# Performance work log

Hardware: AMD Instinct MI355X
Metric: run time of the kernel (lower is better)

## Reference

```python
import jax, jax.numpy as jnp
import numpy as np

N = 100000   # nodes
E = 1600000  # edges
D_IN = 7
H1 = 64
H2 = 32
G = 64       # graphs in batch


def setup_inputs() -> dict:
    key = jax.random.key(0)
    ks = jax.random.split(key, 10)
    x = jax.random.normal(ks[0], (N, D_IN), jnp.float32)
    edge_index = jax.random.randint(ks[1], (2, E), 0, N, dtype=jnp.int64)
    batch = jnp.sort(jax.random.randint(ks[2], (N,), 0, G, dtype=jnp.int64))
    # Glorot-style init for GCN weights
    W1 = jax.random.normal(ks[3], (D_IN, H1), jnp.float32) * (1.0 / np.sqrt(D_IN))
    b1 = jnp.zeros((H1,), jnp.float32)
    W2 = jax.random.normal(ks[4], (H1, H2), jnp.float32) * (1.0 / np.sqrt(H1))
    b2 = jnp.zeros((H2,), jnp.float32)
    W3 = jax.random.normal(ks[5], (H1, H2), jnp.float32) * (1.0 / np.sqrt(H1))
    b3 = jnp.zeros((H2,), jnp.float32)
    eps = jax.random.normal(ks[6], (N, H2), jnp.float32)  # reparam noise
    return dict(x=x, edge_index=edge_index, batch=batch,
                W1=W1, b1=b1, W2=W2, b2=b2, W3=W3, b3=b3, eps=eps)


def _gcn_agg(xw, src, dst, dis):
    # Symmetric-normalized aggregation with self-loops (PyG GCNConv default):
    # out[i] = sum_{(j->i)} d_i^{-1/2} d_j^{-1/2} xw[j] + d_i^{-1} xw[i]
    norm = (dis[src] * dis[dst])[:, None]
    msg = xw[src] * norm                      # [E, H] gather
    out = jax.ops.segment_sum(msg, dst, num_segments=N)  # scatter-add
    return out + xw * (dis * dis)[:, None]    # self-loop term


def reference(x, edge_index, batch, W1, b1, W2, b2, W3, b3, eps):
    src, dst = edge_index[0], edge_index[1]
    # degree on A + I (targets), unit edge weights
    deg = jax.ops.segment_sum(jnp.ones((E,), x.dtype), dst, num_segments=N) + 1.0
    dis = jax.lax.rsqrt(deg)  # deg^{-1/2}

    hidden1 = jax.nn.relu(_gcn_agg(x @ W1, src, dst, dis) + b1)

    # global mean pool of raw x over graphs
    counts = jax.ops.segment_sum(jnp.ones((N,), x.dtype), batch, num_segments=G)
    x_pooled = jax.ops.segment_sum(x, batch, num_segments=G) / jnp.maximum(counts, 1.0)[:, None]

    mu = jax.nn.relu(_gcn_agg(hidden1 @ W2, src, dst, dis) + b2)
    logvar = jax.nn.relu(_gcn_agg(hidden1 @ W3, src, dst, dis) + b3)

    # reparameterize: std = exp(logvar) (no 0.5 factor, as in source)
    z = eps * jnp.exp(logvar) + mu
    return z, x_pooled, mu, logvar
```

## Files before the change

### kernel.cpp

```cpp
#include <hip/hip_runtime.h>
#include <hip/hip_bf16.h>
#include <hip/hip_fp16.h>

#define NN 100000
#define NE 1600000
#define D_IN 7
#define H1 64
#define H2 32
#define NG 64
#define TE 2048
#define NTILE 782
#define BSH 9
#define NBUK 196
#define CAP 10240

typedef _Float16 f16x8 __attribute__((ext_vector_type(8)));
typedef float f32x4 __attribute__((ext_vector_type(4)));

__device__ int lower_bound_i(const int* a, int n, int v) {
    int lo = 0, hi = n;
    while (lo < hi) { int mid = (lo + hi) >> 1; if (a[mid] < v) lo = mid + 1; else hi = mid; }
    return lo;
}

__global__ void k_pi(const float* __restrict__ x, const int* __restrict__ batch,
                     float* __restrict__ outp, int* __restrict__ bucket_cursor) {
    int g = blockIdx.x, t = threadIdx.x;
    if (g == NG) {
        if (t < 256) bucket_cursor[t] = t * CAP;
        return;
    }
    __shared__ int bounds[2];
    __shared__ float red[256 * D_IN];
    if (t == 0) {
        bounds[0] = lower_bound_i(batch, NN, g);
        bounds[1] = lower_bound_i(batch, NN, g + 1);
    }
    __syncthreads();
    int s = bounds[0], e = bounds[1];
    float acc[D_IN];
#pragma unroll
    for (int k = 0; k < D_IN; k++) acc[k] = 0.f;
    for (int n = s + t; n < e; n += 256) {
#pragma unroll
        for (int k = 0; k < D_IN; k++) acc[k] += x[n * D_IN + k];
    }
#pragma unroll
    for (int k = 0; k < D_IN; k++) red[t * D_IN + k] = acc[k];
    __syncthreads();
    if (t < D_IN) {
        float sum = 0.f;
        for (int i = 0; i < 256; i++) sum += red[i * D_IN + t];
        float cnt = (float)(e - s);
        outp[g * D_IN + t] = sum / fmaxf(cnt, 1.f);
    }
}

__global__ __launch_bounds__(256) void k_bin(const int* __restrict__ src,
                                             const int* __restrict__ dst,
                                             int* __restrict__ bucket_cursor,
                                             int* __restrict__ staging) {
    __shared__ int hist[NBUK];
    __shared__ int startx[NBUK];
    __shared__ int runb[NBUK];
    __shared__ int cur[NBUK];
    __shared__ int wsum[4];
    __shared__ int2 pairs[TE];
    int t = threadIdx.x;
    int base = blockIdx.x * TE;
    int tile_cnt = min(TE, NE - base);
    for (int i = t; i < NBUK; i += 256) hist[i] = 0;
    __syncthreads();
    int myd[TE / 256], mys[TE / 256];
#pragma unroll
    for (int k = 0; k < TE / 256; k++) {
        int i = base + k * 256 + t;
        if (i < NE) {
            myd[k] = dst[i]; mys[k] = src[i];
            atomicAdd(&hist[myd[k] >> BSH], 1);
        } else myd[k] = -1;
    }
    __syncthreads();
    int hv = (t < NBUK) ? hist[t] : 0;
    int lane = t & 63, wv = t >> 6;
    int sv = hv;
#pragma unroll
    for (int off = 1; off < 64; off <<= 1) {
        int n = __shfl_up(sv, off, 64);
        if (lane >= off) sv += n;
    }
    if (lane == 63) wsum[wv] = sv;
    __syncthreads();
    int wbase = 0;
#pragma unroll
    for (int i = 0; i < 4; i++) wbase += (i < wv) ? wsum[i] : 0;
    if (t < NBUK) {
        int ex = wbase + sv - hv;
        startx[t] = ex;
        cur[t] = ex;
        if (hv > 0) runb[t] = atomicAdd(&bucket_cursor[t], hv);
    }
    __syncthreads();
#pragma unroll
    for (int k = 0; k < TE / 256; k++) {
        if (myd[k] >= 0) {
            int b = myd[k] >> BSH;
            int slot = atomicAdd(&cur[b], 1);
            pairs[slot] = make_int2(myd[k], mys[k]);
        }
    }
    __syncthreads();
    for (int i = t; i < tile_cnt; i += 256) {
        int2 p = pairs[i];
        int b = p.x >> BSH;
        staging[runb[b] + (i - startx[b])] = ((p.x & 511) << 17) | p.y;
    }
}

__global__ __launch_bounds__(512) void k_build(const int* __restrict__ staging,
                                               const int* __restrict__ bucket_cursor,
                                               int2* __restrict__ rowinfo,
                                               float* __restrict__ dis,
                                               int* __restrict__ csr,
                                               const float* __restrict__ x,
                                               float* __restrict__ xd8) {
    __shared__ int cnt[512];
    __shared__ int cur[512];
    __shared__ int wsum[8];
    int t = threadIdx.x;
    int nbase = blockIdx.x << BSH;
    int ebase = blockIdx.x * CAP;
    int eend = bucket_cursor[blockIdx.x];
    cnt[t] = 0;
    __syncthreads();
    for (int i = ebase + t; i < eend; i += 512)
        atomicAdd(&cnt[staging[i] >> 17], 1);
    __syncthreads();
    int v = cnt[t];
    int lane = t & 63, wv = t >> 6;
    int sv = v;
#pragma unroll
    for (int off = 1; off < 64; off <<= 1) {
        int n = __shfl_up(sv, off, 64);
        if (lane >= off) sv += n;
    }
    if (lane == 63) wsum[wv] = sv;
    __syncthreads();
    int wbase = 0;
#pragma unroll
    for (int i = 0; i < 8; i++) wbase += (i < wv) ? wsum[i] : 0;
    int excl = wbase + sv - v;
    cur[t] = excl;
    int node = nbase + t;
    if (node < NN) {
        rowinfo[node] = make_int2(ebase + excl, v);
        float d = rsqrtf((float)v + 1.0f);
        dis[node] = d;
        const float* xr = x + (size_t)node * D_IN;
        float4 w0 = make_float4(d * xr[0], d * xr[1], d * xr[2], d * xr[3]);
        float4 w1 = make_float4(d * xr[4], d * xr[5], d * xr[6], 0.f);
        float4* xo = (float4*)(xd8 + (size_t)node * 8);
        xo[0] = w0; xo[1] = w1;
    }
    __syncthreads();
    for (int i = ebase + t; i < eend; i += 512) {
        int p = staging[i];
        int pos = ebase + atomicAdd(&cur[p >> 17], 1);
        csr[pos] = p & 0x1FFFF;
    }
}

__global__ __launch_bounds__(256) void k_aggx(const int2* __restrict__ rowinfo,
                                              const float* __restrict__ dis,
                                              const int* __restrict__ csr,
                                              const float* __restrict__ xd8,
                                              const float* __restrict__ W1,
                                              const float* __restrict__ b1,
                                              __half* __restrict__ h1h) {
    __shared__ float sW[D_IN * H1];
    __shared__ float sb[H1];
    __shared__ float sAx[64 * 9];
    int t = threadIdx.x;
    for (int i = t; i < D_IN * H1; i += 256) sW[i] = W1[i];
    if (t < H1) sb[t] = b1[t];
    int ll = t & 3;
    int ln = t >> 2;
    int node = blockIdx.x * 64 + ln;
    int nodec = min(node, NN - 1);
    int2 ri = rowinfo[nodec];
    int start = ri.x, c = ri.y;
    int cpos = start + max(c - 1, 0);
    int cmax = c;
    cmax = max(cmax, __shfl_xor(cmax, 4, 64));
    cmax = max(cmax, __shfl_xor(cmax, 8, 64));
    cmax = max(cmax, __shfl_xor(cmax, 16, 64));
    cmax = max(cmax, __shfl_xor(cmax, 32, 64));
    const float2* xb = (const float2*)xd8;
    float2 acc[4];
#pragma unroll
    for (int k = 0; k < 4; k++) acc[k] = make_float2(0.f, 0.f);
    for (int j = 0; j < cmax; j += 16) {
#pragma unroll
        for (int k = 0; k < 16; k++) {
            bool v = (j + k) < c;
            int s = csr[min(start + j + k, cpos)];
            s = v ? s : nodec;
            float2 r = xb[(size_t)s * 4 + ll];
            acc[k & 3].x += v ? r.x : 0.f;
            acc[k & 3].y += v ? r.y : 0.f;
        }
    }
    float sx = acc[0].x + acc[1].x + acc[2].x + acc[3].x;
    float sy = acc[0].y + acc[1].y + acc[2].y + acc[3].y;
    float2 self = xb[(size_t)nodec * 4 + ll];
    float dn = dis[nodec];
    sAx[ln * 9 + 2 * ll]     = dn * (sx + self.x);
    sAx[ln * 9 + 2 * ll + 1] = dn * (sy + self.y);
    __syncthreads();
    if (node < NN) {
        const float* axp = &sAx[ln * 9];
        union { __half h[16]; float4 f[2]; } u;
#pragma unroll
        for (int j = 0; j < 16; j++) {
            int h = ll * 16 + j;
            float a = sb[h];
#pragma unroll
            for (int k = 0; k < D_IN; k++) a += axp[k] * sW[k * H1 + h];
            u.h[j] = __float2half(dn * fmaxf(a, 0.f));
        }
        float4* d4 = (float4*)(h1h + (size_t)node * H1 + ll * 16);
        d4[0] = u.f[0];
        d4[1] = u.f[1];
    }
}

__device__ __forceinline__ void pk_acc4(__half2* a, float4 r, bool v) {
    unsigned u0 = v ? *reinterpret_cast<unsigned*>(&r.x) : 0u;
    unsigned u1 = v ? *reinterpret_cast<unsigned*>(&r.y) : 0u;
    unsigned u2 = v ? *reinterpret_cast<unsigned*>(&r.z) : 0u;
    unsigned u3 = v ? *reinterpret_cast<unsigned*>(&r.w) : 0u;
    a[0] = __hadd2(a[0], *reinterpret_cast<__half2*>(&u0));
    a[1] = __hadd2(a[1], *reinterpret_cast<__half2*>(&u1));
    a[2] = __hadd2(a[2], *reinterpret_cast<__half2*>(&u2));
    a[3] = __hadd2(a[3], *reinterpret_cast<__half2*>(&u3));
}

__global__ __launch_bounds__(256) void k_agg2f(const int2* __restrict__ rowinfo,
                                               const float* __restrict__ dis,
                                               const int* __restrict__ csr,
                                               const __half* __restrict__ h1h,
                                               const float* __restrict__ W2,
                                               const float* __restrict__ W3,
                                               const float* __restrict__ b2,
                                               const float* __restrict__ b3,
                                               const float* __restrict__ eps,
                                               float* __restrict__ out_z,
                                               float* __restrict__ out_mu,
                                               float* __restrict__ out_lv) {
    __shared__ __align__(16) _Float16 sW[64 * 80];
    __shared__ __align__(16) _Float16 sT[64 * 72];
    int t = threadIdx.x;
    for (int i = t; i < 64 * 64; i += 256) {
        int c = i >> 6, k = i & 63;
        float w = (c < 32) ? W2[k * H2 + c] : W3[k * H2 + (c - 32)];
        sW[c * 80 + k] = (_Float16)w;
    }
    int lane = t & 63;
    int wv = t >> 6;
    int l7 = lane & 7, sub8 = lane >> 3;
    const float4* yb4 = (const float4*)h1h;
    for (int g = 0; g < 2; g++) {
        int lrow = wv * 16 + g * 8 + sub8;
        int node = blockIdx.x * 64 + lrow;
        int nodec = min(node, NN - 1);
        int2 ri = rowinfo[nodec];
        int start = ri.x, c = ri.y;
        int cpos = start + max(c - 1, 0);
        int cmax = c;
        cmax = max(cmax, __shfl_xor(cmax, 8, 64));
        cmax = max(cmax, __shfl_xor(cmax, 16, 64));
        cmax = max(cmax, __shfl_xor(cmax, 32, 64));
        __half2 z2 = __float2half2_rn(0.f);
        __half2 acc[4][4];
#pragma unroll
        for (int i = 0; i < 4; i++)
#pragma unroll
            for (int k = 0; k < 4; k++) acc[i][k] = z2;
        for (int j = 0; j < cmax; j += 16) {
#pragma unroll
            for (int k = 0; k < 16; k++) {
                bool v = (j + k) < c;
                int s = csr[min(start + j + k, cpos)];
                s = v ? s : nodec;
                float4 r = yb4[(size_t)s * 8 + l7];
                pk_acc4(acc[k & 3], r, v);
            }
        }
        __half2 s0 = __hadd2(__hadd2(acc[0][0], acc[1][0]), __hadd2(acc[2][0], acc[3][0]));
        __half2 s1 = __hadd2(__hadd2(acc[0][1], acc[1][1]), __hadd2(acc[2][1], acc[3][1]));
        __half2 s2 = __hadd2(__hadd2(acc[0][2], acc[1][2]), __hadd2(acc[2][2], acc[3][2]));
        __half2 s3 = __hadd2(__hadd2(acc[0][3], acc[1][3]), __hadd2(acc[2][3], acc[3][3]));
        float4 selfv = yb4[(size_t)nodec * 8 + l7];
        __half2* sh = reinterpret_cast<__half2*>(&selfv);
        float dn = dis[nodec];
        float2 f0 = __half22float2(s0), e0 = __half22float2(sh[0]);
        float2 f1 = __half22float2(s1), e1 = __half22float2(sh[1]);
        float2 f2 = __half22float2(s2), e2 = __half22float2(sh[2]);
        float2 f3 = __half22float2(s3), e3 = __half22float2(sh[3]);
        __half2 o0, o1, o2, o3;
        o0.x = __float2half(dn * (f0.x + e0.x)); o0.y = __float2half(dn * (f0.y + e0.y));
        o1.x = __float2half(dn * (f1.x + e1.x)); o1.y = __float2half(dn * (f1.y + e1.y));
        o2.x = __float2half(dn * (f2.x + e2.x)); o2.y = __float2half(dn * (f2.y + e2.y));
        o3.x = __float2half(dn * (f3.x + e3.x)); o3.y = __float2half(dn * (f3.y + e3.y));
        float4 st;
        st.x = *reinterpret_cast<float*>(&o0);
        st.y = *reinterpret_cast<float*>(&o1);
        st.z = *reinterpret_cast<float*>(&o2);
        st.w = *reinterpret_cast<float*>(&o3);
        *(float4*)&sT[lrow * 72 + l7 * 8] = st;
    }
    __syncthreads();
    int sub = lane >> 4, l15 = lane & 15;
    int c15 = l15, k8 = sub;
    const _Float16* ap = &sT[(wv * 16 + c15) * 72];
    f16x8 a0 = *(const f16x8*)(ap + k8 * 8);
    f16x8 a1 = *(const f16x8*)(ap + 32 + k8 * 8);
    const _Float16* wb = sW + (size_t)c15 * 80 + k8 * 8;
    f16x8 b00 = *(const f16x8*)(wb);
    f16x8 b01 = *(const f16x8*)(wb + 32);
    f16x8 b10 = *(const f16x8*)(wb + 16 * 80);
    f16x8 b11 = *(const f16x8*)(wb + 16 * 80 + 32);
    f16x8 b20 = *(const f16x8*)(wb + 32 * 80);
    f16x8 b21 = *(const f16x8*)(wb + 32 * 80 + 32);
    f16x8 b30 = *(const f16x8*)(wb + 48 * 80);
    f16x8 b31 = *(const f16x8*)(wb + 48 * 80 + 32);
    f32x4 ac0 = {0.f, 0.f, 0.f, 0.f};
    f32x4 ac1 = ac0, ac2 = ac0, ac3 = ac0;
    ac0 = __builtin_amdgcn_mfma_f32_16x16x32_f16(a0, b00, ac0, 0, 0, 0);
    ac0 = __builtin_amdgcn_mfma_f32_16x16x32_f16(a1, b01, ac0, 0, 0, 0);
    ac1 = __builtin_amdgcn_mfma_f32_16x16x32_f16(a0, b10, ac1, 0, 0, 0);
    ac1 = __builtin_amdgcn_mfma_f32_16x16x32_f16(a1, b11, ac1, 0, 0, 0);
    ac2 = __builtin_amdgcn_mfma_f32_16x16x32_f16(a0, b20, ac2, 0, 0, 0);
    ac2 = __builtin_amdgcn_mfma_f32_16x16x32_f16(a1, b21, ac2, 0, 0, 0);
    ac3 = __builtin_amdgcn_mfma_f32_16x16x32_f16(a0, b30, ac3, 0, 0, 0);
    ac3 = __builtin_amdgcn_mfma_f32_16x16x32_f16(a1, b31, ac3, 0, 0, 0);
    float bb2a = b2[c15], bb2b = b2[c15 + 16];
    float bb3a = b3[c15], bb3b = b3[c15 + 16];
    int srow = blockIdx.x * 64 + wv * 16 + k8 * 4;
#pragma unroll
    for (int i = 0; i < 4; i++) {
        int r = srow + i;
        if (r < NN) {
            float mu0 = fmaxf(ac0[i] + bb2a, 0.f);
            float mu1 = fmaxf(ac1[i] + bb2b, 0.f);
            float lv0 = fmaxf(ac2[i] + bb3a, 0.f);
            float lv1 = fmaxf(ac3[i] + bb3b, 0.f);
            size_t o0 = (size_t)r * 32 + c15;
            float e0 = eps[o0], e1 = eps[o0 + 16];
            out_mu[o0]      = mu0;
            out_mu[o0 + 16] = mu1;
            out_lv[o0]      = lv0;
            out_lv[o0 + 16] = lv1;
            out_z[o0]       = e0 * __expf(lv0) + mu0;
            out_z[o0 + 16]  = e1 * __expf(lv1) + mu1;
        }
    }
}

extern "C" void kernel_launch(void* const* d_in, const int* in_sizes, int n_in,
                              void* d_out, int out_size, void* d_ws, size_t ws_size,
                              hipStream_t stream) {
    const float* x   = (const float*)d_in[0];
    const int*   ei  = (const int*)d_in[1];
    const int*   bat = (const int*)d_in[2];
    const float* W1  = (const float*)d_in[3];
    const float* b1  = (const float*)d_in[4];
    const float* W2  = (const float*)d_in[5];
    const float* b2  = (const float*)d_in[6];
    const float* W3  = (const float*)d_in[7];
    const float* b3  = (const float*)d_in[8];
    const float* eps = (const float*)d_in[9];

    const int* src = ei;
    const int* dst = ei + NE;

    float* out = (float*)d_out;
    float* out_z    = out;
    float* out_pool = out + (size_t)NN * H2;
    float* out_mu   = out_pool + NG * D_IN;
    float* out_lv   = out_mu + (size_t)NN * H2;

    int*    bucket_cursor = (int*)d_ws;
    int2*   rowinfo       = (int2*)(bucket_cursor + 256);
    float*  dis           = (float*)(rowinfo + NN);
    int*    staging       = (int*)(dis + NN);
    int*    csr           = staging + (size_t)NBUK * CAP;
    __half* h1h           = (__half*)(csr + (size_t)NBUK * CAP);
    float*  xd8           = (float*)(h1h + (size_t)NN * H1);

    k_pi    <<<NG + 1, 256, 0, stream>>>(x, bat, out_pool, bucket_cursor);
    k_bin   <<<NTILE, 256, 0, stream>>>(src, dst, bucket_cursor, staging);
    k_build <<<NBUK, 512, 0, stream>>>(staging, bucket_cursor, rowinfo, dis, csr, x, xd8);
    k_aggx  <<<(NN + 63) / 64, 256, 0, stream>>>(rowinfo, dis, csr, xd8, W1, b1, h1h);
    k_agg2f <<<(NN + 63) / 64, 256, 0, stream>>>(rowinfo, dis, csr, h1h, W2, W3,
                                                 b2, b3, eps, out_z, out_mu, out_lv);
}
```

Measured before the change: 205.8 us.

## Slice hidden features by column, aggregate per slice, split GEMM into separate kernel

Stores hidden1 in a column-sliced layout (8 slices of 8 halves per node) and replaces the fused aggregate+MFMA kernel with a per-slice aggregation kernel, where one thread owns one node and one slice, plus a separate MFMA kernel that reads the aggregated slices. Consecutive block indices cycle through the 8 slices of the same node range, so the gather working set per pass is 1/8 of the feature table and should fit better in cache. It also removes the per-wave max-degree loop padding and uses nontemporal loads and stores for streamed data. The cost is an extra kernel launch and a round trip of the aggregated features through global memory.

New measurement: 308.9 us. 1.5x slower.

```diff
diff --git a/kernel.cpp b/kernel.cpp
--- a/kernel.cpp
+++ b/kernel.cpp
@@ -176,7 +176,7 @@
                                               const float* __restrict__ xd8,
                                               const float* __restrict__ W1,
                                               const float* __restrict__ b1,
-                                              __half* __restrict__ h1h) {
+                                              __half* __restrict__ h1s) {
     __shared__ float sW[D_IN * H1];
     __shared__ float sb[H1];
     __shared__ float sAx[64 * 9];
@@ -228,103 +228,106 @@
             for (int k = 0; k < D_IN; k++) a += axp[k] * sW[k * H1 + h];
             u.h[j] = __float2half(dn * fmaxf(a, 0.f));
         }
-        float4* d4 = (float4*)(h1h + (size_t)node * H1 + ll * 16);
-        d4[0] = u.f[0];
-        d4[1] = u.f[1];
-    }
-}
-
-__device__ __forceinline__ void pk_acc4(__half2* a, float4 r, bool v) {
-    unsigned u0 = v ? *reinterpret_cast<unsigned*>(&r.x) : 0u;
-    unsigned u1 = v ? *reinterpret_cast<unsigned*>(&r.y) : 0u;
-    unsigned u2 = v ? *reinterpret_cast<unsigned*>(&r.z) : 0u;
-    unsigned u3 = v ? *reinterpret_cast<unsigned*>(&r.w) : 0u;
-    a[0] = __hadd2(a[0], *reinterpret_cast<__half2*>(&u0));
-    a[1] = __hadd2(a[1], *reinterpret_cast<__half2*>(&u1));
-    a[2] = __hadd2(a[2], *reinterpret_cast<__half2*>(&u2));
-    a[3] = __hadd2(a[3], *reinterpret_cast<__half2*>(&u3));
-}
-
-__global__ __launch_bounds__(256) void k_agg2f(const int2* __restrict__ rowinfo,
+        *(float4*)(h1s + ((size_t)(2 * ll)     * NN + node) * 8) = u.f[0];
+        *(float4*)(h1s + ((size_t)(2 * ll + 1) * NN + node) * 8) = u.f[1];
+    }
+}
+
+union v16u {
+    f32x4 v;
+    unsigned u[4];
+    __half2 h[4];
+};
+
+__device__ __forceinline__ void pk_acc4t(__half2 a[4][4], int k, f32x4 r, bool v) {
+    v16u w; w.v = r;
+    unsigned u0 = v ? w.u[0] : 0u;
+    unsigned u1 = v ? w.u[1] : 0u;
+    unsigned u2 = v ? w.u[2] : 0u;
+    unsigned u3 = v ? w.u[3] : 0u;
+    a[k][0] = __hadd2(a[k][0], *reinterpret_cast<__half2*>(&u0));
+    a[k][1] = __hadd2(a[k][1], *reinterpret_cast<__half2*>(&u1));
+    a[k][2] = __hadd2(a[k][2], *reinterpret_cast<__half2*>(&u2));
+    a[k][3] = __hadd2(a[k][3], *reinterpret_cast<__half2*>(&u3));
+}
+
+__global__ __launch_bounds__(256) void k_agg2s(const int2* __restrict__ rowinfo,
                                                const float* __restrict__ dis,
                                                const int* __restrict__ csr,
-                                               const __half* __restrict__ h1h,
-                                               const float* __restrict__ W2,
-                                               const float* __restrict__ W3,
-                                               const float* __restrict__ b2,
-                                               const float* __restrict__ b3,
-                                               const float* __restrict__ eps,
-                                               float* __restrict__ out_z,
-                                               float* __restrict__ out_mu,
-                                               float* __restrict__ out_lv) {
+                                               const __half* __restrict__ h1s,
+                                               __half* __restrict__ sAgg) {
+    int t = threadIdx.x;
+    int sl = blockIdx.x & 7;
+    int nb = blockIdx.x >> 3;
+    int node = nb * 256 + t;
+    int nodec = min(node, NN - 1);
+    long long rll = __builtin_nontemporal_load(
+        reinterpret_cast<const long long*>(&rowinfo[nodec]));
+    int start = (int)(rll & 0xFFFFFFFFll);
+    int c     = (int)(rll >> 32);
+    int cpos = start + max(c - 1, 0);
+    const f32x4* tb = (const f32x4*)(h1s + (size_t)sl * NN * 8);
+    __half2 z2 = __float2half2_rn(0.f);
+    __half2 acc[4][4];
+#pragma unroll
+    for (int i = 0; i < 4; i++)
+#pragma unroll
+        for (int k = 0; k < 4; k++) acc[i][k] = z2;
+    for (int j = 0; j < c; j += 16) {
+#pragma unroll
+        for (int k = 0; k < 16; k++) {
+            bool v = (j + k) < c;
+            int s = __builtin_nontemporal_load(&csr[min(start + j + k, cpos)]);
+            s = v ? s : nodec;
+            f32x4 r = tb[s];
+            pk_acc4t(acc, k & 3, r, v);
+        }
+    }
+    __half2 s0 = __hadd2(__hadd2(acc[0][0], acc[1][0]), __hadd2(acc[2][0], acc[3][0]));
+    __half2 s1 = __hadd2(__hadd2(acc[0][1], acc[1][1]), __hadd2(acc[2][1], acc[3][1]));
+    __half2 s2 = __hadd2(__hadd2(acc[0][2], acc[1][2]), __hadd2(acc[2][2], acc[3][2]));
+    __half2 s3 = __hadd2(__hadd2(acc[0][3], acc[1][3]), __hadd2(acc[2][3], acc[3][3]));
+    v16u sw; sw.v = tb[nodec];
+    float dn = dis[nodec];
+    float2 f0 = __half22float2(s0), e0 = __half22float2(sw.h[0]);
+    float2 f1 = __half22float2(s1), e1 = __half22float2(sw.h[1]);
+    float2 f2 = __half22float2(s2), e2 = __half22float2(sw.h[2]);
+    float2 f3 = __half22float2(s3), e3 = __half22float2(sw.h[3]);
+    v16u ow;
+    ow.h[0].x = __float2half(dn * (f0.x + e0.x)); ow.h[0].y = __float2half(dn * (f0.y + e0.y));
+    ow.h[1].x = __float2half(dn * (f1.x + e1.x)); ow.h[1].y = __float2half(dn * (f1.y + e1.y));
+    ow.h[2].x = __float2half(dn * (f2.x + e2.x)); ow.h[2].y = __float2half(dn * (f2.y + e2.y));
+    ow.h[3].x = __float2half(dn * (f3.x + e3.x)); ow.h[3].y = __float2half(dn * (f3.y + e3.y));
+    if (node < NN) {
+        __builtin_nontemporal_store(ow.v, (f32x4*)(sAgg + ((size_t)sl * NN + node) * 8));
+    }
+}
+
+__global__ __launch_bounds__(256) void k_mm23(const __half* __restrict__ sAgg,
+                                              const float* __restrict__ W2,
+                                              const float* __restrict__ W3,
+                                              const float* __restrict__ b2,
+                                              const float* __restrict__ b3,
+                                              const float* __restrict__ eps,
+                                              float* __restrict__ out_z,
+                                              float* __restrict__ out_mu,
+                                              float* __restrict__ out_lv) {
     __shared__ __align__(16) _Float16 sW[64 * 80];
-    __shared__ __align__(16) _Float16 sT[64 * 72];
     int t = threadIdx.x;
     for (int i = t; i < 64 * 64; i += 256) {
         int c = i >> 6, k = i & 63;
         float w = (c < 32) ? W2[k * H2 + c] : W3[k * H2 + (c - 32)];
         sW[c * 80 + k] = (_Float16)w;
     }
+    __syncthreads();
     int lane = t & 63;
     int wv = t >> 6;
-    int l7 = lane & 7, sub8 = lane >> 3;
-    const float4* yb4 = (const float4*)h1h;
-    for (int g = 0; g < 2; g++) {
-        int lrow = wv * 16 + g * 8 + sub8;
-        int node = blockIdx.x * 64 + lrow;
-        int nodec = min(node, NN - 1);
-        int2 ri = rowinfo[nodec];
-        int start = ri.x, c = ri.y;
-        int cpos = start + max(c - 1, 0);
-        int cmax = c;
-        cmax = max(cmax, __shfl_xor(cmax, 8, 64));
-        cmax = max(cmax, __shfl_xor(cmax, 16, 64));
-        cmax = max(cmax, __shfl_xor(cmax, 32, 64));
-        __half2 z2 = __float2half2_rn(0.f);
-        __half2 acc[4][4];
-#pragma unroll
-        for (int i = 0; i < 4; i++)
-#pragma unroll
-            for (int k = 0; k < 4; k++) acc[i][k] = z2;
-        for (int j = 0; j < cmax; j += 16) {
-#pragma unroll
-            for (int k = 0; k < 16; k++) {
-                bool v = (j + k) < c;
-                int s = csr[min(start + j + k, cpos)];
-                s = v ? s : nodec;
-                float4 r = yb4[(size_t)s * 8 + l7];
-                pk_acc4(acc[k & 3], r, v);
-            }
-        }
-        __half2 s0 = __hadd2(__hadd2(acc[0][0], acc[1][0]), __hadd2(acc[2][0], acc[3][0]));
-        __half2 s1 = __hadd2(__hadd2(acc[0][1], acc[1][1]), __hadd2(acc[2][1], acc[3][1]));
-        __half2 s2 = __hadd2(__hadd2(acc[0][2], acc[1][2]), __hadd2(acc[2][2], acc[3][2]));
-        __half2 s3 = __hadd2(__hadd2(acc[0][3], acc[1][3]), __hadd2(acc[2][3], acc[3][3]));
-        float4 selfv = yb4[(size_t)nodec * 8 + l7];
-        __half2* sh = reinterpret_cast<__half2*>(&selfv);
-        float dn = dis[nodec];
-        float2 f0 = __half22float2(s0), e0 = __half22float2(sh[0]);
-        float2 f1 = __half22float2(s1), e1 = __half22float2(sh[1]);
-        float2 f2 = __half22float2(s2), e2 = __half22float2(sh[2]);
-        float2 f3 = __half22float2(s3), e3 = __half22float2(sh[3]);
-        __half2 o0, o1, o2, o3;
-        o0.x = __float2half(dn * (f0.x + e0.x)); o0.y = __float2half(dn * (f0.y + e0.y));
-        o1.x = __float2half(dn * (f1.x + e1.x)); o1.y = __float2half(dn * (f1.y + e1.y));
-        o2.x = __float2half(dn * (f2.x + e2.x)); o2.y = __float2half(dn * (f2.y + e2.y));
-        o3.x = __float2half(dn * (f3.x + e3.x)); o3.y = __float2half(dn * (f3.y + e3.y));
-        float4 st;
-        st.x = *reinterpret_cast<float*>(&o0);
-        st.y = *reinterpret_cast<float*>(&o1);
-        st.z = *reinterpret_cast<float*>(&o2);
-        st.w = *reinterpret_cast<float*>(&o3);
-        *(float4*)&sT[lrow * 72 + l7 * 8] = st;
-    }
-    __syncthreads();
     int sub = lane >> 4, l15 = lane & 15;
     int c15 = l15, k8 = sub;
-    const _Float16* ap = &sT[(wv * 16 + c15) * 72];
-    f16x8 a0 = *(const f16x8*)(ap + k8 * 8);
-    f16x8 a1 = *(const f16x8*)(ap + 32 + k8 * 8);
+    int r0 = blockIdx.x * 64 + wv * 16;
+    int rowc = min(r0 + c15, NN - 1);
+    f16x8 a0 = *(const f16x8*)(sAgg + ((size_t)k8 * NN + rowc) * 8);
+    f16x8 a1 = *(const f16x8*)(sAgg + ((size_t)(k8 + 4) * NN + rowc) * 8);
     const _Float16* wb = sW + (size_t)c15 * 80 + k8 * 8;
     f16x8 b00 = *(const f16x8*)(wb);
     f16x8 b01 = *(const f16x8*)(wb + 32);
@@ -346,7 +349,7 @@
     ac3 = __builtin_amdgcn_mfma_f32_16x16x32_f16(a1, b31, ac3, 0, 0, 0);
     float bb2a = b2[c15], bb2b = b2[c15 + 16];
     float bb3a = b3[c15], bb3b = b3[c15 + 16];
-    int srow = blockIdx.x * 64 + wv * 16 + k8 * 4;
+    int srow = r0 + k8 * 4;
 #pragma unroll
     for (int i = 0; i < 4; i++) {
         int r = srow + i;
@@ -395,13 +398,15 @@
     float*  dis           = (float*)(rowinfo + NN);
     int*    staging       = (int*)(dis + NN);
     int*    csr           = staging + (size_t)NBUK * CAP;
-    __half* h1h           = (__half*)(csr + (size_t)NBUK * CAP);
-    float*  xd8           = (float*)(h1h + (size_t)NN * H1);
+    __half* h1s           = (__half*)(csr + (size_t)NBUK * CAP);
+    float*  xd8           = (float*)(h1s + (size_t)NN * H1);
+    __half* sAgg          = (__half*)(xd8 + (size_t)NN * 8);
 
     k_pi    <<<NG + 1, 256, 0, stream>>>(x, bat, out_pool, bucket_cursor);
     k_bin   <<<NTILE, 256, 0, stream>>>(src, dst, bucket_cursor, staging);
     k_build <<<NBUK, 512, 0, stream>>>(staging, bucket_cursor, rowinfo, dis, csr, x, xd8);
-    k_aggx  <<<(NN + 63) / 64, 256, 0, stream>>>(rowinfo, dis, csr, xd8, W1, b1, h1h);
-    k_agg2f <<<(NN + 63) / 64, 256, 0, stream>>>(rowinfo, dis, csr, h1h, W2, W3,
-                                                 b2, b3, eps, out_z, out_mu, out_lv);
-}
+    k_aggx  <<<(NN + 63) / 64, 256, 0, stream>>>(rowinfo, dis, csr, xd8, W1, b1, h1s);
+    k_agg2s <<<8 * ((NN + 255) / 256), 256, 0, stream>>>(rowinfo, dis, csr, h1s, sAgg);
+    k_mm23  <<<(NN + 63) / 64, 256, 0, stream>>>(sAgg, W2, W3, b2, b3, eps,
+                                                 out_z, out_mu, out_lv);
+}
```
